# Optimization experiments

Measured on AMD Instinct MI355X. Metric: run time of the kernel, lower is better.

Reference implementation:

```python
import jax, jax.numpy as jnp
import numpy as np

N_NODES = 100000
N_EDGES = 640000
D_IN = 128
D_OUT = 128


def setup_inputs() -> dict:
    key = jax.random.key(0)
    k1, k2, k3, k4, k5 = jax.random.split(key, 5)
    feats = jax.random.normal(k1, (N_NODES, D_IN), dtype=jnp.float32)
    src = jax.random.randint(k2, (N_EDGES,), 0, N_NODES, dtype=jnp.int32)
    dst = jax.random.randint(k3, (N_EDGES,), 0, N_NODES, dtype=jnp.int32)
    # Xavier-normal-ish init (gain for relu = sqrt(2))
    std = float(np.sqrt(2.0) * np.sqrt(2.0 / (D_IN + D_OUT)))
    linear_skip_weight = jax.random.normal(k4, (D_OUT, D_IN), dtype=jnp.float32) * std
    linear_msg_weight = jax.random.normal(k5, (D_OUT, D_IN), dtype=jnp.float32) * std
    linear_skip_bias = jnp.zeros((D_OUT,), dtype=jnp.float32)
    linear_msg_bias = jnp.zeros((D_OUT,), dtype=jnp.float32)
    return {
        "feats": feats,
        "src": src,
        "dst": dst,
        "linear_skip_weight": linear_skip_weight,
        "linear_skip_bias": linear_skip_bias,
        "linear_msg_weight": linear_msg_weight,
        "linear_msg_bias": linear_msg_bias,
    }


def reference(feats, src, dst, linear_skip_weight, linear_skip_bias,
              linear_msg_weight, linear_msg_bias):
    n = feats.shape[0]
    # degree from scatter-add of edge weights (ones) at source rows
    deg = jax.ops.segment_sum(jnp.ones_like(src, dtype=feats.dtype), src,
                              num_segments=n)
    deg_inv_sqrt = jnp.where(deg > 0, jax.lax.rsqrt(jnp.maximum(deg, 1.0)) * (deg > 0), 0.0)
    deg_inv_sqrt = jnp.where(deg > 0, deg ** -0.5, 0.0)
    # normalize source features, gather along edges, scatter-sum to dst
    feat_src = feats * deg_inv_sqrt[:, None]           # [N, D_IN]
    msgs = feat_src[src]                               # [E, D_IN]
    rst = jax.ops.segment_sum(msgs, dst, num_segments=n)  # [N, D_IN]
    rst = rst * deg_inv_sqrt[:, None]
    rst_ = rst @ linear_msg_weight.T + linear_msg_bias
    skip_x = feats @ linear_skip_weight.T + linear_skip_bias
    return rst_ + skip_x
```

## Files before the change

kernel.cpp:

```cpp
#include <hip/hip_runtime.h>

#define N_NODES 100000
#define N_EDGES 640000
#define D 128
#define NB ((N_NODES + 1023) / 1024)
#define BKT_C 16
#define OVF_CAP 32768

typedef short v8s __attribute__((ext_vector_type(8)));
typedef float v4f __attribute__((ext_vector_type(4)));
typedef unsigned int v4u __attribute__((ext_vector_type(4)));
typedef int v4i __attribute__((ext_vector_type(4)));

__device__ __forceinline__ unsigned short f2bf(float x) {
    unsigned int u = __builtin_bit_cast(unsigned int, x);
    u += 0x7fffu + ((u >> 16) & 1u);
    return (unsigned short)(u >> 16);
}
__device__ __forceinline__ float bf2f(unsigned int hi) {
    return __builtin_bit_cast(float, hi << 16);
}

__global__ __launch_bounds__(256) void k_zero(int4* __restrict__ pk4,
                                              int4* __restrict__ bkt4,
                                              int* __restrict__ ovf_cnt) {
    int i = blockIdx.x * blockDim.x + threadIdx.x;
    if (i < N_NODES / 4) pk4[i] = make_int4(0, 0, 0, 0);
    if (bkt4 && i < N_NODES * BKT_C / 4) bkt4[i] = make_int4(0, 0, 0, 0);
    if (i == 0 && ovf_cnt) *ovf_cnt = 0;
}

__global__ __launch_bounds__(256) void k_pre(const float* __restrict__ feats,
                                             const float* __restrict__ Wm,
                                             const float* __restrict__ Ws,
                                             const float* __restrict__ bmsg,
                                             const float* __restrict__ bskip,
                                             const int* __restrict__ src,
                                             const int* __restrict__ dst,
                                             unsigned int* __restrict__ pk,
                                             unsigned short* __restrict__ Bcat,
                                             float* __restrict__ bias,
                                             char* __restrict__ fsbase,
                                             int fs_stride,
                                             int* __restrict__ bucket,
                                             int* __restrict__ ovf_cnt,
                                             int2* __restrict__ ovf) {
    int i = blockIdx.x * blockDim.x + threadIdx.x;
    if (i < D * D) {
        int j = i >> 7;
        int k = i & 127;
        Bcat[j * 256 + k]       = f2bf(Wm[i]);
        Bcat[j * 256 + 128 + k] = f2bf(Ws[i]);
    }
    if (i < D) bias[i] = bmsg[i] + bskip[i];
    if (i < N_EDGES) {
        int s = __builtin_nontemporal_load(&src[i]);
        int d = __builtin_nontemporal_load(&dst[i]);
        atomicAdd(&pk[s], 1u);
        unsigned int old = atomicAdd(&pk[d], 0x10000u);
        if (bucket) {
            unsigned int p = old >> 16;
            if (p < BKT_C) {
                bucket[d * BKT_C + (int)p] = s;
            } else {
                int q = atomicAdd(ovf_cnt, 1);
                if (q < OVF_CAP) ovf[q] = make_int2(d, s);
            }
        }
    }
    int g = i * 8;
    int row = g >> 7;
    int col = g & 127;
    if (row < N_NODES) {
        const v4f* sp = (const v4f*)(feats + g);
        v4f x = __builtin_nontemporal_load(sp);
        v4f y = __builtin_nontemporal_load(sp + 1);
        v4u p;
        p.x = (unsigned)f2bf(x.x) | ((unsigned)f2bf(x.y) << 16);
        p.y = (unsigned)f2bf(x.z) | ((unsigned)f2bf(x.w) << 16);
        p.z = (unsigned)f2bf(y.x) | ((unsigned)f2bf(y.y) << 16);
        p.w = (unsigned)f2bf(y.z) | ((unsigned)f2bf(y.w) << 16);
        __builtin_nontemporal_store(p, (v4u*)(fsbase + (size_t)row * fs_stride + col * 2));
    }
}

__global__ __launch_bounds__(256) void k_agg_c(char* __restrict__ outb,
                                               const char* __restrict__ featsh,
                                               const unsigned int* __restrict__ pk,
                                               const int* __restrict__ bucket,
                                               const int* __restrict__ ovf_cnt,
                                               const int2* __restrict__ ovf) {
    int wid = (int)((blockIdx.x * (unsigned)blockDim.x + threadIdx.x) >> 6);
    int lane = threadIdx.x & 63;
    if (wid >= N_NODES) return;
    int grp = lane >> 4;
    int sub = lane & 15;

    v4i bq = __builtin_nontemporal_load((const v4i*)(bucket + wid * BKT_C + grp * 4));
    unsigned int pkn = pk[wid];

    int sA = bq.x, sB = bq.y, sC = bq.z, sD = bq.w;
    unsigned int pA = pk[sA];
    unsigned int pB = pk[sB];
    unsigned int pC = pk[sC];
    unsigned int pD = pk[sD];
    uint4 vA = *(const uint4*)(featsh + (size_t)sA * 256 + sub * 16);
    uint4 vB = *(const uint4*)(featsh + (size_t)sB * 256 + sub * 16);
    uint4 vC = *(const uint4*)(featsh + (size_t)sC * 256 + sub * 16);
    uint4 vD = *(const uint4*)(featsh + (size_t)sD * 256 + sub * 16);

    int cnt = (int)(pkn >> 16);
    int m = cnt < BKT_C ? cnt : BKT_C;
    int e0 = grp * 4;
    float gA = (e0 < m) ? 1.0f : 0.0f;
    float gB = (e0 + 1 < m) ? 1.0f : 0.0f;
    float gC = (e0 + 2 < m) ? 1.0f : 0.0f;
    float gD = (e0 + 3 < m) ? 1.0f : 0.0f;

    float scA = gA * rsqrtf(fmaxf((float)(pA & 0xffffu), 1.0f));
    float scB = gB * rsqrtf(fmaxf((float)(pB & 0xffffu), 1.0f));
    float scC = gC * rsqrtf(fmaxf((float)(pC & 0xffffu), 1.0f));
    float scD = gD * rsqrtf(fmaxf((float)(pD & 0xffffu), 1.0f));

    float acc[8];
#pragma unroll
    for (int i = 0; i < 8; i++) acc[i] = 0.f;
    acc[0] += bf2f(vA.x & 0xffffu) * scA; acc[1] += bf2f(vA.x >> 16) * scA;
    acc[2] += bf2f(vA.y & 0xffffu) * scA; acc[3] += bf2f(vA.y >> 16) * scA;
    acc[4] += bf2f(vA.z & 0xffffu) * scA; acc[5] += bf2f(vA.z >> 16) * scA;
    acc[6] += bf2f(vA.w & 0xffffu) * scA; acc[7] += bf2f(vA.w >> 16) * scA;
    acc[0] += bf2f(vB.x & 0xffffu) * scB; acc[1] += bf2f(vB.x >> 16) * scB;
    acc[2] += bf2f(vB.y & 0xffffu) * scB; acc[3] += bf2f(vB.y >> 16) * scB;
    acc[4] += bf2f(vB.z & 0xffffu) * scB; acc[5] += bf2f(vB.z >> 16) * scB;
    acc[6] += bf2f(vB.w & 0xffffu) * scB; acc[7] += bf2f(vB.w >> 16) * scB;
    acc[0] += bf2f(vC.x & 0xffffu) * scC; acc[1] += bf2f(vC.x >> 16) * scC;
    acc[2] += bf2f(vC.y & 0xffffu) * scC; acc[3] += bf2f(vC.y >> 16) * scC;
    acc[4] += bf2f(vC.z & 0xffffu) * scC; acc[5] += bf2f(vC.z >> 16) * scC;
    acc[6] += bf2f(vC.w & 0xffffu) * scC; acc[7] += bf2f(vC.w >> 16) * scC;
    acc[0] += bf2f(vD.x & 0xffffu) * scD; acc[1] += bf2f(vD.x >> 16) * scD;
    acc[2] += bf2f(vD.y & 0xffffu) * scD; acc[3] += bf2f(vD.y >> 16) * scD;
    acc[4] += bf2f(vD.z & 0xffffu) * scD; acc[5] += bf2f(vD.z >> 16) * scD;
    acc[6] += bf2f(vD.w & 0xffffu) * scD; acc[7] += bf2f(vD.w >> 16) * scD;

    if (cnt > BKT_C) {
        int no = *ovf_cnt;
        if (no > OVF_CAP) no = OVF_CAP;
        for (int i = grp; i < no; i += 4) {
            int2 p = ovf[i];
            if (p.x == wid) {
                float sc = rsqrtf((float)(pk[p.y] & 0xffffu));
                uint4 v = *(const uint4*)(featsh + (size_t)p.y * 256 + sub * 16);
                acc[0] += bf2f(v.x & 0xffffu) * sc; acc[1] += bf2f(v.x >> 16) * sc;
                acc[2] += bf2f(v.y & 0xffffu) * sc; acc[3] += bf2f(v.y >> 16) * sc;
                acc[4] += bf2f(v.z & 0xffffu) * sc; acc[5] += bf2f(v.z >> 16) * sc;
                acc[6] += bf2f(v.w & 0xffffu) * sc; acc[7] += bf2f(v.w >> 16) * sc;
            }
        }
    }

#pragma unroll
    for (int i = 0; i < 8; i++) {
        acc[i] += __shfl_xor(acc[i], 16);
        acc[i] += __shfl_xor(acc[i], 32);
    }
    if (grp == 0) {
        int dsrc = (int)(pkn & 0xffffu);
        float scn = (dsrc > 0) ? rsqrtf((float)dsrc) : 0.0f;
        v4u p;
        p.x = (unsigned)f2bf(acc[0] * scn) | ((unsigned)f2bf(acc[1] * scn) << 16);
        p.y = (unsigned)f2bf(acc[2] * scn) | ((unsigned)f2bf(acc[3] * scn) << 16);
        p.z = (unsigned)f2bf(acc[4] * scn) | ((unsigned)f2bf(acc[5] * scn) << 16);
        p.w = (unsigned)f2bf(acc[6] * scn) | ((unsigned)f2bf(acc[7] * scn) << 16);
        __builtin_nontemporal_store(p, (v4u*)(outb + (size_t)wid * 512 + sub * 16));
    }
}

__global__ __launch_bounds__(256) void k_gemm_c(const char* __restrict__ featsh,
                                                const unsigned short* __restrict__ Bcat,
                                                const float* __restrict__ bias,
                                                float* __restrict__ outf) {
    __shared__ unsigned short Bl[128][264];
    const char* Ab = (const char*)outf;
    int tid = threadIdx.x;
    int lane = tid & 63;
    int w = tid >> 6;
    int n0 = blockIdx.x * 128;

    for (int i = tid; i < 128 * 32; i += 256) {
        int r = i >> 5, c = i & 31;
        *(uint4*)(&Bl[r][c * 8]) = *(const uint4*)(Bcat + r * 256 + c * 8);
    }
    __syncthreads();

    int q = lane >> 4;
    int lr = lane & 15;

    int r0 = n0 + w * 32 + lr;      if (r0 > N_NODES - 1) r0 = N_NODES - 1;
    int r1 = n0 + w * 32 + 16 + lr; if (r1 > N_NODES - 1) r1 = N_NODES - 1;
    const char* g0p = Ab + (size_t)r0 * 512 + q * 16;
    const char* g1p = Ab + (size_t)r1 * 512 + q * 16;
    const char* f0p = featsh + (size_t)r0 * 256 + q * 16;
    const char* f1p = featsh + (size_t)r1 * 256 + q * 16;

    v4f acc[2][8];
#pragma unroll
    for (int mt = 0; mt < 2; mt++)
#pragma unroll
        for (int t = 0; t < 8; t++) acc[mt][t] = (v4f){0.f, 0.f, 0.f, 0.f};

#pragma unroll
    for (int kk = 0; kk < 8; kk++) {
        v8s a0, a1;
        if (kk < 4) {
            a0 = __builtin_nontemporal_load((const v8s*)(g0p + kk * 64));
            a1 = __builtin_nontemporal_load((const v8s*)(g1p + kk * 64));
        } else {
            a0 = __builtin_nontemporal_load((const v8s*)(f0p + (kk - 4) * 64));
            a1 = __builtin_nontemporal_load((const v8s*)(f1p + (kk - 4) * 64));
        }
#pragma unroll
        for (int t = 0; t < 8; t++) {
            v8s b = *(const v8s*)(&Bl[t * 16 + lr][kk * 32 + q * 8]);
            acc[0][t] = __builtin_amdgcn_mfma_f32_16x16x32_bf16(a0, b, acc[0][t], 0, 0, 0);
            acc[1][t] = __builtin_amdgcn_mfma_f32_16x16x32_bf16(a1, b, acc[1][t], 0, 0, 0);
        }
    }

#pragma unroll
    for (int t = 0; t < 8; t++) {
        float bv = bias[t * 16 + lr];
#pragma unroll
        for (int mt = 0; mt < 2; mt++) {
            int rowb = n0 + w * 32 + mt * 16 + q * 4;
#pragma unroll
            for (int r = 0; r < 4; r++) {
                int row = rowb + r;
                if (row < N_NODES)
                    __builtin_nontemporal_store(acc[mt][t][r] + bv,
                        &outf[(size_t)row * 128 + t * 16 + lr]);
            }
        }
    }
}

__device__ __forceinline__ void agg_edge(const char* outb,
                                         const unsigned int* pk,
                                         int s, int sub, float* acc) {
    float sc = rsqrtf((float)(pk[s] & 0xffffu));
    uint4 v = *(const uint4*)(outb + (size_t)s * 512 + 256 + sub * 16);
    acc[0] += bf2f(v.x & 0xffffu) * sc;
    acc[1] += bf2f(v.x >> 16) * sc;
    acc[2] += bf2f(v.y & 0xffffu) * sc;
    acc[3] += bf2f(v.y >> 16) * sc;
    acc[4] += bf2f(v.z & 0xffffu) * sc;
    acc[5] += bf2f(v.z >> 16) * sc;
    acc[6] += bf2f(v.w & 0xffffu) * sc;
    acc[7] += bf2f(v.w >> 16) * sc;
}

__device__ __forceinline__ void agg_acc(uint4 v, float sc, float* acc) {
    acc[0] += bf2f(v.x & 0xffffu) * sc;
    acc[1] += bf2f(v.x >> 16) * sc;
    acc[2] += bf2f(v.y & 0xffffu) * sc;
    acc[3] += bf2f(v.y >> 16) * sc;
    acc[4] += bf2f(v.z & 0xffffu) * sc;
    acc[5] += bf2f(v.z >> 16) * sc;
    acc[6] += bf2f(v.w & 0xffffu) * sc;
    acc[7] += bf2f(v.w >> 16) * sc;
}

__device__ __forceinline__ void agg_finish(char* outb, int wid,
                                           unsigned int pkn, int grp, int sub,
                                           float* acc) {
#pragma unroll
    for (int i = 0; i < 8; i++) {
        acc[i] += __shfl_xor(acc[i], 16);
        acc[i] += __shfl_xor(acc[i], 32);
    }
    if (grp == 0) {
        int dsrc = (int)(pkn & 0xffffu);
        float scn = (dsrc > 0) ? rsqrtf((float)dsrc) : 0.0f;
        uint4 p;
        p.x = (unsigned)f2bf(acc[0] * scn) | ((unsigned)f2bf(acc[1] * scn) << 16);
        p.y = (unsigned)f2bf(acc[2] * scn) | ((unsigned)f2bf(acc[3] * scn) << 16);
        p.z = (unsigned)f2bf(acc[4] * scn) | ((unsigned)f2bf(acc[5] * scn) << 16);
        p.w = (unsigned)f2bf(acc[6] * scn) | ((unsigned)f2bf(acc[7] * scn) << 16);
        *(uint4*)(outb + (size_t)wid * 512 + sub * 16) = p;
    }
}

__global__ __launch_bounds__(256) void k_agg_bkt(char* __restrict__ outb,
                                                 const unsigned int* __restrict__ pk,
                                                 const int* __restrict__ bucket,
                                                 const int* __restrict__ ovf_cnt,
                                                 const int2* __restrict__ ovf) {
    int wid = (int)((blockIdx.x * (unsigned)blockDim.x + threadIdx.x) >> 6);
    int lane = threadIdx.x & 63;
    if (wid >= N_NODES) return;
    int grp = lane >> 4;
    int sub = lane & 15;
    unsigned int pkn = pk[wid];
    int cnt = (int)(pkn >> 16);
    int m = cnt < BKT_C ? cnt : BKT_C;
    const int* bk = bucket + wid * BKT_C;

    int4 bq = *(const int4*)(bk + grp * 4);
    int e0 = grp * 4;

    bool a0 = e0 < m, a1 = e0 + 1 < m, a2 = e0 + 2 < m, a3 = e0 + 3 < m;
    int sA = a0 ? bq.x : 0; float gA = a0 ? 1.0f : 0.0f;
    int sB = a1 ? bq.y : 0; float gB = a1 ? 1.0f : 0.0f;
    int sC = a2 ? bq.z : 0; float gC = a2 ? 1.0f : 0.0f;
    int sD = a3 ? bq.w : 0; float gD = a3 ? 1.0f : 0.0f;

    unsigned int pA = pk[sA];
    unsigned int pB = pk[sB];
    unsigned int pC = pk[sC];
    unsigned int pD = pk[sD];
    uint4 vA = *(const uint4*)(outb + (size_t)sA * 512 + 256 + sub * 16);
    uint4 vB = *(const uint4*)(outb + (size_t)sB * 512 + 256 + sub * 16);
    uint4 vC = *(const uint4*)(outb + (size_t)sC * 512 + 256 + sub * 16);
    uint4 vD = *(const uint4*)(outb + (size_t)sD * 512 + 256 + sub * 16);

    float scA = gA * rsqrtf(fmaxf((float)(pA & 0xffffu), 1.0f));
    float scB = gB * rsqrtf(fmaxf((float)(pB & 0xffffu), 1.0f));
    float scC = gC * rsqrtf(fmaxf((float)(pC & 0xffffu), 1.0f));
    float scD = gD * rsqrtf(fmaxf((float)(pD & 0xffffu), 1.0f));

    float acc[8];
#pragma unroll
    for (int i = 0; i < 8; i++) acc[i] = 0.f;
    agg_acc(vA, scA, acc);
    agg_acc(vB, scB, acc);
    agg_acc(vC, scC, acc);
    agg_acc(vD, scD, acc);

    if (cnt > BKT_C) {
        int no = *ovf_cnt;
        if (no > OVF_CAP) no = OVF_CAP;
        for (int i = grp; i < no; i += 4) {
            int2 p = ovf[i];
            if (p.x == wid) agg_edge(outb, pk, p.y, sub, acc);
        }
    }
    agg_finish(outb, wid, pkn, grp, sub, acc);
}

__global__ __launch_bounds__(256) void k_scan1(const unsigned int* __restrict__ pk,
                                               int* __restrict__ rowptr,
                                               int* __restrict__ bsums) {
    __shared__ int sd[256];
    int t = threadIdx.x;
    int i0 = blockIdx.x * 1024 + t * 4;
    int v[4];
    int s = 0;
#pragma unroll
    for (int q = 0; q < 4; q++) {
        int i = i0 + q;
        v[q] = (i < N_NODES) ? (int)(pk[i] >> 16) : 0;
        s += v[q];
    }
    sd[t] = s;
    __syncthreads();
    for (int off = 1; off < 256; off <<= 1) {
        int y = (t >= off) ? sd[t - off] : 0;
        __syncthreads();
        sd[t] += y;
        __syncthreads();
    }
    int run = sd[t] - s;
    if (t == 255) bsums[blockIdx.x] = sd[255];
#pragma unroll
    for (int q = 0; q < 4; q++) {
        int i = i0 + q;
        if (i < N_NODES) rowptr[i] = run;
        run += v[q];
    }
}

__global__ __launch_bounds__(128) void k_scan2(int* __restrict__ bsums) {
    __shared__ int sd[128];
    int t = threadIdx.x;
    int v = (t < NB) ? bsums[t] : 0;
    sd[t] = v;
    __syncthreads();
    for (int off = 1; off < 128; off <<= 1) {
        int y = (t >= off) ? sd[t - off] : 0;
        __syncthreads();
        sd[t] += y;
        __syncthreads();
    }
    if (t < NB) bsums[t] = sd[t] - v;
}

__global__ __launch_bounds__(256) void k_scan3(const int* __restrict__ bsums,
                                               int* __restrict__ rowptr) {
    int add = bsums[blockIdx.x];
    int i0 = blockIdx.x * 1024 + threadIdx.x * 4;
#pragma unroll
    for (int q = 0; q < 4; q++) {
        int i = i0 + q;
        if (i < N_NODES) rowptr[i] += add;
    }
}

__global__ __launch_bounds__(256) void k_fill(const int* __restrict__ src,
                                              const int* __restrict__ dst,
                                              int* __restrict__ rowptr,
                                              int* __restrict__ csr_src) {
    int e = blockIdx.x * blockDim.x + threadIdx.x;
    if (e < N_EDGES) {
        int p = atomicAdd(&rowptr[dst[e]], 1);
        csr_src[p] = src[e];
    }
}

__global__ __launch_bounds__(256) void k_agg_csr(char* __restrict__ outb,
                                                 const unsigned int* __restrict__ pk,
                                                 const int* __restrict__ rowptr,
                                                 const int* __restrict__ csr_src) {
    int wid = (int)((blockIdx.x * (unsigned)blockDim.x + threadIdx.x) >> 6);
    int lane = threadIdx.x & 63;
    if (wid >= N_NODES) return;
    int grp = lane >> 4;
    int sub = lane & 15;
    int start = (wid == 0) ? 0 : rowptr[wid - 1];
    int end = rowptr[wid];
    float acc[8];
#pragma unroll
    for (int i = 0; i < 8; i++) acc[i] = 0.f;
    for (int base = start; base < end; base += 4) {
        int e = base + grp;
        if (e < end) agg_edge(outb, pk, csr_src[e], sub, acc);
    }
    agg_finish(outb, wid, pk[wid], grp, sub, acc);
}

__global__ __launch_bounds__(256) void k_gemm(const unsigned short* __restrict__ Bcat,
                                              const float* __restrict__ bias,
                                              float* __restrict__ outf) {
    __shared__ unsigned short Bl[128][264];
    const char* Ab = (const char*)outf;
    int tid = threadIdx.x;
    int lane = tid & 63;
    int w = tid >> 6;
    int n0 = blockIdx.x * 128;

    for (int i = tid; i < 128 * 32; i += 256) {
        int r = i >> 5, c = i & 31;
        *(uint4*)(&Bl[r][c * 8]) = *(const uint4*)(Bcat + r * 256 + c * 8);
    }
    __syncthreads();

    int q = lane >> 4;
    int lr = lane & 15;

    int r0 = n0 + w * 32 + lr;      if (r0 > N_NODES - 1) r0 = N_NODES - 1;
    int r1 = n0 + w * 32 + 16 + lr; if (r1 > N_NODES - 1) r1 = N_NODES - 1;
    const char* a0p = Ab + (size_t)r0 * 512 + q * 16;
    const char* a1p = Ab + (size_t)r1 * 512 + q * 16;

    v4f acc[2][8];
#pragma unroll
    for (int mt = 0; mt < 2; mt++)
#pragma unroll
        for (int t = 0; t < 8; t++) acc[mt][t] = (v4f){0.f, 0.f, 0.f, 0.f};

#pragma unroll
    for (int kk = 0; kk < 8; kk++) {
        v8s a0 = *(const v8s*)(a0p + kk * 64);
        v8s a1 = *(const v8s*)(a1p + kk * 64);
#pragma unroll
        for (int t = 0; t < 8; t++) {
            v8s b = *(const v8s*)(&Bl[t * 16 + lr][kk * 32 + q * 8]);
            acc[0][t] = __builtin_amdgcn_mfma_f32_16x16x32_bf16(a0, b, acc[0][t], 0, 0, 0);
            acc[1][t] = __builtin_amdgcn_mfma_f32_16x16x32_bf16(a1, b, acc[1][t], 0, 0, 0);
        }
    }

#pragma unroll
    for (int t = 0; t < 8; t++) {
        float bv = bias[t * 16 + lr];
#pragma unroll
        for (int mt = 0; mt < 2; mt++) {
            int rowb = n0 + w * 32 + mt * 16 + q * 4;
#pragma unroll
            for (int r = 0; r < 4; r++) {
                int row = rowb + r;
                if (row < N_NODES)
                    outf[(size_t)row * 128 + t * 16 + lr] = acc[mt][t][r] + bv;
            }
        }
    }
}

extern "C" void kernel_launch(void* const* d_in, const int* in_sizes, int n_in,
                              void* d_out, int out_size, void* d_ws, size_t ws_size,
                              hipStream_t stream) {
    const float* feats = (const float*)d_in[0];
    const int*   src   = (const int*)d_in[1];
    const int*   dst   = (const int*)d_in[2];
    const float* Wskip = (const float*)d_in[3];
    const float* bskip = (const float*)d_in[4];
    const float* Wmsg  = (const float*)d_in[5];
    const float* bmsg  = (const float*)d_in[6];

    char* w = (char*)d_ws;

    bool pathC = ws_size >= (size_t)32728320;
    bool pathA = ws_size >= (size_t)7128320;

    if (pathC) {
        unsigned int*   pk      = (unsigned int*)w;
        int*            ovf_cnt = (int*)(w + 400000);
        unsigned short* Bcat    = (unsigned short*)(w + 400128);
        float*          bias    = (float*)(w + 465664);
        int*            bucket  = (int*)(w + 466176);
        int2*           ovf     = (int2*)(w + 6866176);
        char*           featsh  = w + 7128320;

        hipLaunchKernelGGL(k_zero, dim3((N_NODES * BKT_C / 4 + 255) / 256),
                           dim3(256), 0, stream, (int4*)pk, (int4*)bucket, ovf_cnt);
        hipLaunchKernelGGL(k_pre, dim3((N_NODES * (D / 8) + 255) / 256), dim3(256),
                           0, stream, feats, Wmsg, Wskip, bmsg, bskip, src, dst, pk,
                           Bcat, bias, featsh, 256, bucket, ovf_cnt, ovf);
        hipLaunchKernelGGL(k_agg_c, dim3((N_NODES * 64 + 255) / 256), dim3(256), 0,
                           stream, (char*)d_out, featsh, pk, bucket, ovf_cnt, ovf);
        hipLaunchKernelGGL(k_gemm_c, dim3((N_NODES + 127) / 128), dim3(256), 0,
                           stream, featsh, Bcat, bias, (float*)d_out);
    } else if (pathA) {
        unsigned int*   pk      = (unsigned int*)w;
        int*            ovf_cnt = (int*)(w + 400000);
        unsigned short* Bcat    = (unsigned short*)(w + 400128);
        float*          bias    = (float*)(w + 465664);
        int*            bucket  = (int*)(w + 466176);
        int2*           ovf     = (int2*)(w + 6866176);

        hipLaunchKernelGGL(k_zero, dim3((N_NODES / 4 + 255) / 256), dim3(256), 0,
                           stream, (int4*)pk, (int4*)nullptr, ovf_cnt);
        hipLaunchKernelGGL(k_pre, dim3((N_NODES * (D / 8) + 255) / 256), dim3(256),
                           0, stream, feats, Wmsg, Wskip, bmsg, bskip, src, dst, pk,
                           Bcat, bias, (char*)d_out + 256, 512, bucket, ovf_cnt, ovf);
        hipLaunchKernelGGL(k_agg_bkt, dim3((N_NODES * 64 + 255) / 256), dim3(256), 0,
                           stream, (char*)d_out, pk, bucket, ovf_cnt, ovf);
        hipLaunchKernelGGL(k_gemm, dim3((N_NODES + 127) / 128), dim3(256), 0, stream,
                           Bcat, bias, (float*)d_out);
    } else {
        unsigned int*   pk      = (unsigned int*)w;
        int*            rowptr  = (int*)(w + 400000);
        int*            bsums   = (int*)(w + 800128);
        unsigned short* Bcat    = (unsigned short*)(w + 800640);
        float*          bias    = (float*)(w + 866176);
        int*            csr_src = (int*)(w + 866688);

        hipLaunchKernelGGL(k_zero, dim3((N_NODES / 4 + 255) / 256), dim3(256), 0,
                           stream, (int4*)pk, (int4*)nullptr, (int*)nullptr);
        hipLaunchKernelGGL(k_pre, dim3((N_NODES * (D / 8) + 255) / 256), dim3(256),
                           0, stream, feats, Wmsg, Wskip, bmsg, bskip, src, dst, pk,
                           Bcat, bias, (char*)d_out + 256, 512, (int*)nullptr,
                           (int*)nullptr, (int2*)nullptr);
        hipLaunchKernelGGL(k_scan1, dim3(NB), dim3(256), 0, stream, pk, rowptr,
                           bsums);
        hipLaunchKernelGGL(k_scan2, dim3(1), dim3(128), 0, stream, bsums);
        hipLaunchKernelGGL(k_scan3, dim3(NB), dim3(256), 0, stream, bsums, rowptr);
        hipLaunchKernelGGL(k_fill, dim3((N_EDGES + 255) / 256), dim3(256), 0, stream,
                           src, dst, rowptr, csr_src);
        hipLaunchKernelGGL(k_agg_csr, dim3((N_NODES * 64 + 255) / 256), dim3(256), 0,
                           stream, (char*)d_out, pk, rowptr, csr_src);
        hipLaunchKernelGGL(k_gemm, dim3((N_NODES + 127) / 128), dim3(256), 0, stream,
                           Bcat, bias, (float*)d_out);
    }
}
```

Before: 236.6 us.

## Fuse neighbor aggregation into the MFMA GEMM kernel via LDS staging

Merges the aggregation kernel and the GEMM kernel into one. Each wave aggregates 16 destination nodes sequentially, writes the bf16 results into shared memory, then uses them as the A operand for MFMA alongside the original features. This removes the global round-trip of the aggregated intermediate and a launch. It also reads the weight matrix directly from global/cache instead of staging it in LDS. The serial per-wave node loop reduces memory-level parallelism for the latency-bound gathers.

```diff
diff --git a/kernel.cpp b/kernel.cpp
--- a/kernel.cpp
+++ b/kernel.cpp
@@ -84,161 +84,141 @@
     }
 }
 
-__global__ __launch_bounds__(256) void k_agg_c(char* __restrict__ outb,
-                                               const char* __restrict__ featsh,
-                                               const unsigned int* __restrict__ pk,
-                                               const int* __restrict__ bucket,
-                                               const int* __restrict__ ovf_cnt,
-                                               const int2* __restrict__ ovf) {
-    int wid = (int)((blockIdx.x * (unsigned)blockDim.x + threadIdx.x) >> 6);
-    int lane = threadIdx.x & 63;
-    if (wid >= N_NODES) return;
-    int grp = lane >> 4;
-    int sub = lane & 15;
-
-    v4i bq = __builtin_nontemporal_load((const v4i*)(bucket + wid * BKT_C + grp * 4));
-    unsigned int pkn = pk[wid];
-
-    int sA = bq.x, sB = bq.y, sC = bq.z, sD = bq.w;
-    unsigned int pA = pk[sA];
-    unsigned int pB = pk[sB];
-    unsigned int pC = pk[sC];
-    unsigned int pD = pk[sD];
-    uint4 vA = *(const uint4*)(featsh + (size_t)sA * 256 + sub * 16);
-    uint4 vB = *(const uint4*)(featsh + (size_t)sB * 256 + sub * 16);
-    uint4 vC = *(const uint4*)(featsh + (size_t)sC * 256 + sub * 16);
-    uint4 vD = *(const uint4*)(featsh + (size_t)sD * 256 + sub * 16);
-
-    int cnt = (int)(pkn >> 16);
-    int m = cnt < BKT_C ? cnt : BKT_C;
-    int e0 = grp * 4;
-    float gA = (e0 < m) ? 1.0f : 0.0f;
-    float gB = (e0 + 1 < m) ? 1.0f : 0.0f;
-    float gC = (e0 + 2 < m) ? 1.0f : 0.0f;
-    float gD = (e0 + 3 < m) ? 1.0f : 0.0f;
-
-    float scA = gA * rsqrtf(fmaxf((float)(pA & 0xffffu), 1.0f));
-    float scB = gB * rsqrtf(fmaxf((float)(pB & 0xffffu), 1.0f));
-    float scC = gC * rsqrtf(fmaxf((float)(pC & 0xffffu), 1.0f));
-    float scD = gD * rsqrtf(fmaxf((float)(pD & 0xffffu), 1.0f));
-
-    float acc[8];
-#pragma unroll
-    for (int i = 0; i < 8; i++) acc[i] = 0.f;
-    acc[0] += bf2f(vA.x & 0xffffu) * scA; acc[1] += bf2f(vA.x >> 16) * scA;
-    acc[2] += bf2f(vA.y & 0xffffu) * scA; acc[3] += bf2f(vA.y >> 16) * scA;
-    acc[4] += bf2f(vA.z & 0xffffu) * scA; acc[5] += bf2f(vA.z >> 16) * scA;
-    acc[6] += bf2f(vA.w & 0xffffu) * scA; acc[7] += bf2f(vA.w >> 16) * scA;
-    acc[0] += bf2f(vB.x & 0xffffu) * scB; acc[1] += bf2f(vB.x >> 16) * scB;
-    acc[2] += bf2f(vB.y & 0xffffu) * scB; acc[3] += bf2f(vB.y >> 16) * scB;
-    acc[4] += bf2f(vB.z & 0xffffu) * scB; acc[5] += bf2f(vB.z >> 16) * scB;
-    acc[6] += bf2f(vB.w & 0xffffu) * scB; acc[7] += bf2f(vB.w >> 16) * scB;
-    acc[0] += bf2f(vC.x & 0xffffu) * scC; acc[1] += bf2f(vC.x >> 16) * scC;
-    acc[2] += bf2f(vC.y & 0xffffu) * scC; acc[3] += bf2f(vC.y >> 16) * scC;
-    acc[4] += bf2f(vC.z & 0xffffu) * scC; acc[5] += bf2f(vC.z >> 16) * scC;
-    acc[6] += bf2f(vC.w & 0xffffu) * scC; acc[7] += bf2f(vC.w >> 16) * scC;
-    acc[0] += bf2f(vD.x & 0xffffu) * scD; acc[1] += bf2f(vD.x >> 16) * scD;
-    acc[2] += bf2f(vD.y & 0xffffu) * scD; acc[3] += bf2f(vD.y >> 16) * scD;
-    acc[4] += bf2f(vD.z & 0xffffu) * scD; acc[5] += bf2f(vD.z >> 16) * scD;
-    acc[6] += bf2f(vD.w & 0xffffu) * scD; acc[7] += bf2f(vD.w >> 16) * scD;
-
-    if (cnt > BKT_C) {
-        int no = *ovf_cnt;
-        if (no > OVF_CAP) no = OVF_CAP;
-        for (int i = grp; i < no; i += 4) {
-            int2 p = ovf[i];
-            if (p.x == wid) {
-                float sc = rsqrtf((float)(pk[p.y] & 0xffffu));
-                uint4 v = *(const uint4*)(featsh + (size_t)p.y * 256 + sub * 16);
-                acc[0] += bf2f(v.x & 0xffffu) * sc; acc[1] += bf2f(v.x >> 16) * sc;
-                acc[2] += bf2f(v.y & 0xffffu) * sc; acc[3] += bf2f(v.y >> 16) * sc;
-                acc[4] += bf2f(v.z & 0xffffu) * sc; acc[5] += bf2f(v.z >> 16) * sc;
-                acc[6] += bf2f(v.w & 0xffffu) * sc; acc[7] += bf2f(v.w >> 16) * sc;
-            }
-        }
-    }
-
-#pragma unroll
-    for (int i = 0; i < 8; i++) {
-        acc[i] += __shfl_xor(acc[i], 16);
-        acc[i] += __shfl_xor(acc[i], 32);
-    }
-    if (grp == 0) {
-        int dsrc = (int)(pkn & 0xffffu);
-        float scn = (dsrc > 0) ? rsqrtf((float)dsrc) : 0.0f;
-        v4u p;
-        p.x = (unsigned)f2bf(acc[0] * scn) | ((unsigned)f2bf(acc[1] * scn) << 16);
-        p.y = (unsigned)f2bf(acc[2] * scn) | ((unsigned)f2bf(acc[3] * scn) << 16);
-        p.z = (unsigned)f2bf(acc[4] * scn) | ((unsigned)f2bf(acc[5] * scn) << 16);
-        p.w = (unsigned)f2bf(acc[6] * scn) | ((unsigned)f2bf(acc[7] * scn) << 16);
-        __builtin_nontemporal_store(p, (v4u*)(outb + (size_t)wid * 512 + sub * 16));
-    }
-}
-
-__global__ __launch_bounds__(256) void k_gemm_c(const char* __restrict__ featsh,
+__global__ __launch_bounds__(512) void k_fused3(const char* __restrict__ featsh,
+                                                const unsigned int* __restrict__ pk,
+                                                const int* __restrict__ bucket,
+                                                const int* __restrict__ ovf_cnt,
+                                                const int2* __restrict__ ovf,
                                                 const unsigned short* __restrict__ Bcat,
                                                 const float* __restrict__ bias,
                                                 float* __restrict__ outf) {
-    __shared__ unsigned short Bl[128][264];
-    const char* Ab = (const char*)outf;
+    __shared__ unsigned short aggh[128][132];
     int tid = threadIdx.x;
     int lane = tid & 63;
     int w = tid >> 6;
     int n0 = blockIdx.x * 128;
-
-    for (int i = tid; i < 128 * 32; i += 256) {
-        int r = i >> 5, c = i & 31;
-        *(uint4*)(&Bl[r][c * 8]) = *(const uint4*)(Bcat + r * 256 + c * 8);
-    }
-    __syncthreads();
-
-    int q = lane >> 4;
-    int lr = lane & 15;
-
-    int r0 = n0 + w * 32 + lr;      if (r0 > N_NODES - 1) r0 = N_NODES - 1;
-    int r1 = n0 + w * 32 + 16 + lr; if (r1 > N_NODES - 1) r1 = N_NODES - 1;
-    const char* g0p = Ab + (size_t)r0 * 512 + q * 16;
-    const char* g1p = Ab + (size_t)r1 * 512 + q * 16;
-    const char* f0p = featsh + (size_t)r0 * 256 + q * 16;
-    const char* f1p = featsh + (size_t)r1 * 256 + q * 16;
-
-    v4f acc[2][8];
-#pragma unroll
-    for (int mt = 0; mt < 2; mt++)
-#pragma unroll
-        for (int t = 0; t < 8; t++) acc[mt][t] = (v4f){0.f, 0.f, 0.f, 0.f};
+    int grp = lane >> 4;
+    int sub = lane & 15;
+
+#pragma unroll 1
+    for (int j = 0; j < 16; ++j) {
+        int wid = n0 + w * 16 + j;
+        int widc = wid < N_NODES ? wid : N_NODES - 1;
+        v4i bq = __builtin_nontemporal_load(
+            (const v4i*)(bucket + widc * BKT_C + grp * 4));
+        unsigned int pkn = pk[widc];
+
+        int sA = bq.x, sB = bq.y, sC = bq.z, sD = bq.w;
+        unsigned int pA = pk[sA];
+        unsigned int pB = pk[sB];
+        unsigned int pC = pk[sC];
+        unsigned int pD = pk[sD];
+        uint4 vA = *(const uint4*)(featsh + (size_t)sA * 256 + sub * 16);
+        uint4 vB = *(const uint4*)(featsh + (size_t)sB * 256 + sub * 16);
+        uint4 vC = *(const uint4*)(featsh + (size_t)sC * 256 + sub * 16);
+        uint4 vD = *(const uint4*)(featsh + (size_t)sD * 256 + sub * 16);
+
+        int cnt = (int)(pkn >> 16);
+        int m = cnt < BKT_C ? cnt : BKT_C;
+        int e0 = grp * 4;
+        float gA = (e0 < m) ? 1.0f : 0.0f;
+        float gB = (e0 + 1 < m) ? 1.0f : 0.0f;
+        float gC = (e0 + 2 < m) ? 1.0f : 0.0f;
+        float gD = (e0 + 3 < m) ? 1.0f : 0.0f;
+
+        float scA = gA * rsqrtf(fmaxf((float)(pA & 0xffffu), 1.0f));
+        float scB = gB * rsqrtf(fmaxf((float)(pB & 0xffffu), 1.0f));
+        float scC = gC * rsqrtf(fmaxf((float)(pC & 0xffffu), 1.0f));
+        float scD = gD * rsqrtf(fmaxf((float)(pD & 0xffffu), 1.0f));
+
+        float acc[8];
+#pragma unroll
+        for (int i = 0; i < 8; i++) acc[i] = 0.f;
+        acc[0] += bf2f(vA.x & 0xffffu) * scA; acc[1] += bf2f(vA.x >> 16) * scA;
+        acc[2] += bf2f(vA.y & 0xffffu) * scA; acc[3] += bf2f(vA.y >> 16) * scA;
+        acc[4] += bf2f(vA.z & 0xffffu) * scA; acc[5] += bf2f(vA.z >> 16) * scA;
+        acc[6] += bf2f(vA.w & 0xffffu) * scA; acc[7] += bf2f(vA.w >> 16) * scA;
+        acc[0] += bf2f(vB.x & 0xffffu) * scB; acc[1] += bf2f(vB.x >> 16) * scB;
+        acc[2] += bf2f(vB.y & 0xffffu) * scB; acc[3] += bf2f(vB.y >> 16) * scB;
+        acc[4] += bf2f(vB.z & 0xffffu) * scB; acc[5] += bf2f(vB.z >> 16) * scB;
+        acc[6] += bf2f(vB.w & 0xffffu) * scB; acc[7] += bf2f(vB.w >> 16) * scB;
+        acc[0] += bf2f(vC.x & 0xffffu) * scC; acc[1] += bf2f(vC.x >> 16) * scC;
+        acc[2] += bf2f(vC.y & 0xffffu) * scC; acc[3] += bf2f(vC.y >> 16) * scC;
+        acc[4] += bf2f(vC.z & 0xffffu) * scC; acc[5] += bf2f(vC.z >> 16) * scC;
+        acc[6] += bf2f(vC.w & 0xffffu) * scC; acc[7] += bf2f(vC.w >> 16) * scC;
+        acc[0] += bf2f(vD.x & 0xffffu) * scD; acc[1] += bf2f(vD.x >> 16) * scD;
+        acc[2] += bf2f(vD.y & 0xffffu) * scD; acc[3] += bf2f(vD.y >> 16) * scD;
+        acc[4] += bf2f(vD.z & 0xffffu) * scD; acc[5] += bf2f(vD.z >> 16) * scD;
+        acc[6] += bf2f(vD.w & 0xffffu) * scD; acc[7] += bf2f(vD.w >> 16) * scD;
+
+        if (cnt > BKT_C) {
+            int no = *ovf_cnt;
+            if (no > OVF_CAP) no = OVF_CAP;
+            for (int i = grp; i < no; i += 4) {
+                int2 p = ovf[i];
+                if (p.x == widc) {
+                    float sc = rsqrtf((float)(pk[p.y] & 0xffffu));
+                    uint4 v = *(const uint4*)(featsh + (size_t)p.y * 256 + sub * 16);
+                    acc[0] += bf2f(v.x & 0xffffu) * sc; acc[1] += bf2f(v.x >> 16) * sc;
+                    acc[2] += bf2f(v.y & 0xffffu) * sc; acc[3] += bf2f(v.y >> 16) * sc;
+                    acc[4] += bf2f(v.z & 0xffffu) * sc; acc[5] += bf2f(v.z >> 16) * sc;
+                    acc[6] += bf2f(v.w & 0xffffu) * sc; acc[7] += bf2f(v.w >> 16) * sc;
+                }
+            }
+        }
+
+#pragma unroll
+        for (int i = 0; i < 8; i++) {
+            acc[i] += __shfl_xor(acc[i], 16);
+            acc[i] += __shfl_xor(acc[i], 32);
+        }
+        if (grp == 0) {
+            int dsrc = (int)(pkn & 0xffffu);
+            float scn = (dsrc > 0) ? rsqrtf((float)dsrc) : 0.0f;
+            uint4 p;
+            p.x = (unsigned)f2bf(acc[0] * scn) | ((unsigned)f2bf(acc[1] * scn) << 16);
+            p.y = (unsigned)f2bf(acc[2] * scn) | ((unsigned)f2bf(acc[3] * scn) << 16);
+            p.z = (unsigned)f2bf(acc[4] * scn) | ((unsigned)f2bf(acc[5] * scn) << 16);
+            p.w = (unsigned)f2bf(acc[6] * scn) | ((unsigned)f2bf(acc[7] * scn) << 16);
+            *(uint4*)(&aggh[w * 16 + j][sub * 8]) = p;
+        }
+    }
+
+    int q = grp;
+    int lr = sub;
+    int r0 = n0 + w * 16 + lr;
+    int r0c = r0 < N_NODES ? r0 : N_NODES - 1;
+    const char* f0p = featsh + (size_t)r0c * 256 + q * 16;
+
+    v4f acc2[8];
+#pragma unroll
+    for (int t = 0; t < 8; t++) acc2[t] = (v4f){0.f, 0.f, 0.f, 0.f};
 
 #pragma unroll
     for (int kk = 0; kk < 8; kk++) {
-        v8s a0, a1;
+        v8s a0;
         if (kk < 4) {
-            a0 = __builtin_nontemporal_load((const v8s*)(g0p + kk * 64));
-            a1 = __builtin_nontemporal_load((const v8s*)(g1p + kk * 64));
+            a0 = *(const v8s*)(&aggh[w * 16 + lr][q * 8 + kk * 32]);
         } else {
             a0 = __builtin_nontemporal_load((const v8s*)(f0p + (kk - 4) * 64));
-            a1 = __builtin_nontemporal_load((const v8s*)(f1p + (kk - 4) * 64));
         }
 #pragma unroll
         for (int t = 0; t < 8; t++) {
-            v8s b = *(const v8s*)(&Bl[t * 16 + lr][kk * 32 + q * 8]);
-            acc[0][t] = __builtin_amdgcn_mfma_f32_16x16x32_bf16(a0, b, acc[0][t], 0, 0, 0);
-            acc[1][t] = __builtin_amdgcn_mfma_f32_16x16x32_bf16(a1, b, acc[1][t], 0, 0, 0);
+            v8s b = *(const v8s*)(Bcat + (t * 16 + lr) * 256 + kk * 32 + q * 8);
+            acc2[t] = __builtin_amdgcn_mfma_f32_16x16x32_bf16(a0, b, acc2[t], 0, 0, 0);
         }
     }
 
 #pragma unroll
     for (int t = 0; t < 8; t++) {
         float bv = bias[t * 16 + lr];
-#pragma unroll
-        for (int mt = 0; mt < 2; mt++) {
-            int rowb = n0 + w * 32 + mt * 16 + q * 4;
-#pragma unroll
-            for (int r = 0; r < 4; r++) {
-                int row = rowb + r;
-                if (row < N_NODES)
-                    __builtin_nontemporal_store(acc[mt][t][r] + bv,
-                        &outf[(size_t)row * 128 + t * 16 + lr]);
-            }
+        int rowb = n0 + w * 16 + q * 4;
+#pragma unroll
+        for (int r = 0; r < 4; r++) {
+            int row = rowb + r;
+            if (row < N_NODES)
+                __builtin_nontemporal_store(acc2[t][r] + bv,
+                    &outf[(size_t)row * 128 + t * 16 + lr]);
         }
     }
 }
@@ -524,10 +504,9 @@
         hipLaunchKernelGGL(k_pre, dim3((N_NODES * (D / 8) + 255) / 256), dim3(256),
                            0, stream, feats, Wmsg, Wskip, bmsg, bskip, src, dst, pk,
                            Bcat, bias, featsh, 256, bucket, ovf_cnt, ovf);
-        hipLaunchKernelGGL(k_agg_c, dim3((N_NODES * 64 + 255) / 256), dim3(256), 0,
-                           stream, (char*)d_out, featsh, pk, bucket, ovf_cnt, ovf);
-        hipLaunchKernelGGL(k_gemm_c, dim3((N_NODES + 127) / 128), dim3(256), 0,
-                           stream, featsh, Bcat, bias, (float*)d_out);
+        hipLaunchKernelGGL(k_fused3, dim3((N_NODES + 127) / 128), dim3(512), 0,
+                           stream, featsh, pk, bucket, ovf_cnt, ovf, Bcat, bias,
+                           (float*)d_out);
     } else if (pathA) {
         unsigned int*   pk      = (unsigned int*)w;
         int*            ovf_cnt = (int*)(w + 400000);
```

Result: slower. 272.1 us (+15.0%).
